# Performance work log

Hardware: AMD Instinct MI355X
Metric: run time of the kernel (lower is better)

The kernel has to match this reference:

```python
import jax, jax.numpy as jnp
import numpy as np

B, C, H, W, N = 32, 256, 56, 56, 1024


def setup_inputs() -> dict:
    key = jax.random.key(0)
    k1, k2, k3, k4 = jax.random.split(key, 4)
    x = jax.random.normal(k1, (B, C, H, W), dtype=jnp.float32)
    W_s = jax.random.normal(k2, (N, H, W), dtype=jnp.float32)
    W_d = jax.random.normal(k3, (N, C, 1, 1), dtype=jnp.float32)
    W_b = jax.random.normal(k4, (1, N), dtype=jnp.float32)
    return {"x": x, "W_s": W_s, "W_d": W_d, "W_b": W_b}


def reference(x, W_s, W_d, W_b):
    # Original: out = einsum('bchw,nhw->bnchw'); per-neuron 1x1 conv with W_d[n]
    # (C -> 1 channel); sum over (c,h,w); add bias. Mathematically:
    #   out[b,n] = sum_{c,h,w} x[b,c,h,w] * W_s[n,h,w] * W_d[n,c] + W_b[0,n]
    # Computed without materializing the (B,N,C,H,W) blow-up:
    y = jnp.einsum('bchw,nhw->bnc', x, W_s)          # spatial contraction
    out = jnp.einsum('bnc,nc->bn', y, W_d[:, :, 0, 0])  # channel contraction
    return out + W_b
```

## Files before the change

kernel.cpp:

```cpp
#include <hip/hip_runtime.h>
#include <stdint.h>


#define K_DIM 3136
#define N_DIM 1024
#define C_DIM 256
#define B_DIM 32
#define M_DIM 8192
#define X_ELEMS (M_DIM * K_DIM)
#define WS_ELEMS (N_DIM * K_DIM)
#define NSTEP 49

typedef __attribute__((ext_vector_type(8))) short short8v;
typedef __attribute__((ext_vector_type(4))) float f32x4;

__device__ __forceinline__ short f2bf(float f) {
  union { float f; unsigned u; } v; v.f = f;
  unsigned r = v.u + 0x7FFFu + ((v.u >> 16) & 1u);
  return (short)(r >> 16);
}

__device__ __forceinline__ void async16(const void* g, void* l) {
  __builtin_amdgcn_global_load_lds(
      (const __attribute__((address_space(1))) unsigned int*)g,
      (__attribute__((address_space(3))) unsigned int*)l, 16, 0, 0);
}

#define XBLK (X_ELEMS / 4096)
#define CVBLK ((X_ELEMS + WS_ELEMS) / 4096)
__global__ __launch_bounds__(256) void convert_bf16_bias(
    const float* __restrict__ x, const float* __restrict__ Ws,
    const float* __restrict__ Wb, short* __restrict__ dst,
    float* __restrict__ out) {
  int bid = blockIdx.x;
  if (bid >= CVBLK) {
    int i = (bid - CVBLK) * 256 + threadIdx.x;
    out[i] = Wb[i & (N_DIM - 1)];
    return;
  }
  const float* src;
  short* d;
  size_t base;
  if (bid < XBLK) {
    src = x; d = dst; base = (size_t)bid * 4096;
  } else {
    src = Ws; d = dst + X_ELEMS; base = (size_t)(bid - XBLK) * 4096;
  }
#pragma unroll
  for (int h = 0; h < 2; ++h) {
    size_t i = base + threadIdx.x * 8 + h * 2048;
    f32x4 v0 = __builtin_nontemporal_load((const f32x4*)(src + i));
    f32x4 v1 = __builtin_nontemporal_load((const f32x4*)(src + i) + 1);
    short8v s;
    s[0] = f2bf(v0.x); s[1] = f2bf(v0.y); s[2] = f2bf(v0.z); s[3] = f2bf(v0.w);
    s[4] = f2bf(v1.x); s[5] = f2bf(v1.y); s[6] = f2bf(v1.z); s[7] = f2bf(v1.w);
    *(short8v*)(d + i) = s;
  }
}


#define VMCNT(N) asm volatile("s_waitcnt vmcnt(" #N ")" ::: "memory")
#define CBAR() asm volatile("" ::: "memory")
#define BARR() { CBAR(); __builtin_amdgcn_s_barrier(); CBAR(); }

#define STAGEA(T) { char* d_ = sm + (((T) & 3) << 15) + (wv << 10);           \
    const short* g_ = Ag + (size_t)(T) * 32;                                  \
    async16(g_, d_);                                                          \
    async16(g_ + (size_t)128 * K_DIM, d_ + 8192); }

#define STAGEB(T) { char* d_ = sm + (((T) & 3) << 15) + 16384 + (wv << 10);   \
    const short* g_ = Bg + (size_t)(T) * 32;                                  \
    async16(g_, d_);                                                          \
    async16(g_ + (size_t)128 * K_DIM, d_ + 8192); }

#define MFQ(F, AV)                                                            \
  acc[F][0] = __builtin_amdgcn_mfma_f32_16x16x32_bf16(AV, b0, acc[F][0], 0, 0, 0); \
  acc[F][1] = __builtin_amdgcn_mfma_f32_16x16x32_bf16(AV, b1, acc[F][1], 0, 0, 0); \
  acc[F][2] = __builtin_amdgcn_mfma_f32_16x16x32_bf16(AV, b2, acc[F][2], 0, 0, 0); \
  acc[F][3] = __builtin_amdgcn_mfma_f32_16x16x32_bf16(AV, b3, acc[F][3], 0, 0, 0);

#define KTILE(T, STG, VMSTMT)                                                 \
  {                                                                           \
    char* sl = sm + (((T) & 3) << 15);                                        \
    if (STG) STAGEA((T) + 3);                                                 \
    short8v b0 = *(const short8v*)(sl + boff);                                \
    short8v b1 = *(const short8v*)(sl + boff + 1024);                         \
    short8v b2 = *(const short8v*)(sl + boff + 2048);                         \
    short8v b3 = *(const short8v*)(sl + boff + 3072);                         \
    short8v a0 = *(const short8v*)(sl + aoff);                                \
    short8v a1 = *(const short8v*)(sl + aoff + 1024);                         \
    short8v a2 = *(const short8v*)(sl + aoff + 2048);                         \
    short8v a3 = *(const short8v*)(sl + aoff + 3072);                         \
    BARR();                                                                   \
    __builtin_amdgcn_s_setprio(1);                                            \
    MFQ(0, a0) MFQ(1, a1) MFQ(2, a2) MFQ(3, a3)                               \
    __builtin_amdgcn_s_setprio(0);                                            \
    BARR();                                                                   \
    if (STG) STAGEB((T) + 3);                                                 \
    a0 = *(const short8v*)(sl + aoff + 4096);                                 \
    a1 = *(const short8v*)(sl + aoff + 5120);                                 \
    a2 = *(const short8v*)(sl + aoff + 6144);                                 \
    a3 = *(const short8v*)(sl + aoff + 7168);                                 \
    VMSTMT;                                                                   \
    __builtin_amdgcn_sched_barrier(0);                                        \
    BARR();                                                                   \
    __builtin_amdgcn_s_setprio(1);                                            \
    MFQ(4, a0) MFQ(5, a1) MFQ(6, a2) MFQ(7, a3)                               \
    __builtin_amdgcn_s_setprio(0);                                            \
    BARR();                                                                   \
  }

__global__ __launch_bounds__(512, 2) void gemm_fused(
    const short* __restrict__ Abf, const short* __restrict__ Bbf,
    const float* __restrict__ Wd, float* __restrict__ out) {
  __shared__ __align__(16) char sm[131072];

  const int bid = blockIdx.x;
  const int xcd = bid & 7;
  const int nt = xcd >> 1;
  const int z = xcd & 1;
  const int mt = bid >> 3;
  const int kt0 = z * NSTEP;

  const int tid = threadIdx.x;
  const int lane = tid & 63;
  const int wv = tid >> 6;
  const int r = lane & 15;
  const int q = lane >> 4;
  const int wm = wv >> 2, wn = wv & 3;

  const int srow = wv * 16 + (lane >> 2);
  const int sk8 = (lane & 3) ^ ((lane >> 3) & 3);
  const short* Ag = Abf + (size_t)(mt * 256 + srow) * K_DIM + kt0 * 32 + sk8 * 8;
  const short* Bg = Bbf + (size_t)(nt * 256 + srow) * K_DIM + kt0 * 32 + sk8 * 8;

  const int swz = (q ^ ((r >> 1) & 3)) << 4;
  const int aoff = (wm * 128 + r) * 64 + swz;
  const int boff = 16384 + (wn * 64 + r) * 64 + swz;

  f32x4 acc[8][4];
#pragma unroll
  for (int i = 0; i < 8; ++i)
#pragma unroll
    for (int j = 0; j < 4; ++j) acc[i][j] = (f32x4)0.0f;

  STAGEA(0) STAGEB(0) STAGEA(1) STAGEB(1) STAGEA(2) STAGEB(2)
  VMCNT(8);
  BARR();

#pragma unroll 1
  for (int t = 0; t < NSTEP - 3; ++t) KTILE(t, 1, VMCNT(8));
  KTILE(NSTEP - 3, 0, VMCNT(4));
  KTILE(NSTEP - 2, 0, VMCNT(0));
  KTILE(NSTEP - 1, 0, (void)0);

#pragma unroll
  for (int j = 0; j < 4; ++j) {
    const int n_g = nt * 256 + wn * 64 + 16 * j + r;
    float p = 0.0f;
#pragma unroll
    for (int i = 0; i < 8; ++i) {
      const int c_l = wm * 128 + 16 * i + 4 * q;
      const float4 wd = *(const float4*)(Wd + (size_t)n_g * C_DIM + c_l);
      p += acc[i][j].x * wd.x + acc[i][j].y * wd.y + acc[i][j].z * wd.z +
           acc[i][j].w * wd.w;
    }
    p += __shfl_xor(p, 16, 64);
    p += __shfl_xor(p, 32, 64);
    if (q == 0) atomicAdd(&out[(size_t)mt * N_DIM + n_g], p);
  }
}

extern "C" void kernel_launch(void* const* d_in, const int* in_sizes, int n_in,
                              void* d_out, int out_size, void* d_ws, size_t ws_size,
                              hipStream_t stream) {
  const float* x = (const float*)d_in[0];
  const float* Ws = (const float*)d_in[1];
  const float* Wd = (const float*)d_in[2];
  const float* Wb = (const float*)d_in[3];
  float* out = (float*)d_out;
  short* xbf = (short*)d_ws;

  convert_bf16_bias<<<dim3(CVBLK + 128), dim3(256), 0, stream>>>(x, Ws, Wb, xbf, out);
  gemm_fused<<<dim3(32 * 4 * 2), dim3(512), 0, stream>>>(xbf, xbf + X_ELEMS, Wd, out);
}
```

Baseline: 212.9 us.

## Fuse x fp32-to-bf16 conversion into GEMM A-tile loading via registers

The separate pre-pass that turned all of x into bf16 in workspace is removed. The GEMM now loads fp32 x rows directly into registers, converts them to bf16 and writes them into swizzled LDS, while B still arrives by async global-to-LDS loads. This drops a full write and re-read of the bf16 copy of x (about 51 MB). In exchange the A tile is loaded at twice the bytes per tile, the software pipeline uses register double-buffering, and the main loop carries more VALU work.

Result: slower. 235.5 us (+10.6%).

```diff
diff --git a/kernel.cpp b/kernel.cpp
--- a/kernel.cpp
+++ b/kernel.cpp
@@ -7,7 +7,6 @@
 #define C_DIM 256
 #define B_DIM 32
 #define M_DIM 8192
-#define X_ELEMS (M_DIM * K_DIM)
 #define WS_ELEMS (N_DIM * K_DIM)
 #define NSTEP 49
 
@@ -26,47 +25,54 @@
       (__attribute__((address_space(3))) unsigned int*)l, 16, 0, 0);
 }
 
-#define XBLK (X_ELEMS / 4096)
-#define CVBLK ((X_ELEMS + WS_ELEMS) / 4096)
-__global__ __launch_bounds__(256) void convert_bf16_bias(
-    const float* __restrict__ x, const float* __restrict__ Ws,
-    const float* __restrict__ Wb, short* __restrict__ dst,
-    float* __restrict__ out) {
+#define WSBLK (WS_ELEMS / 4096)
+__global__ __launch_bounds__(256) void convert_ws_bias(
+    const float* __restrict__ Ws, const float* __restrict__ Wb,
+    short* __restrict__ dst, float* __restrict__ out) {
   int bid = blockIdx.x;
-  if (bid >= CVBLK) {
-    int i = (bid - CVBLK) * 256 + threadIdx.x;
+  if (bid >= WSBLK) {
+    int i = (bid - WSBLK) * 256 + threadIdx.x;
     out[i] = Wb[i & (N_DIM - 1)];
     return;
   }
-  const float* src;
-  short* d;
-  size_t base;
-  if (bid < XBLK) {
-    src = x; d = dst; base = (size_t)bid * 4096;
-  } else {
-    src = Ws; d = dst + X_ELEMS; base = (size_t)(bid - XBLK) * 4096;
-  }
+  size_t base = (size_t)bid * 4096;
 #pragma unroll
   for (int h = 0; h < 2; ++h) {
     size_t i = base + threadIdx.x * 8 + h * 2048;
-    f32x4 v0 = __builtin_nontemporal_load((const f32x4*)(src + i));
-    f32x4 v1 = __builtin_nontemporal_load((const f32x4*)(src + i) + 1);
+    f32x4 v0 = __builtin_nontemporal_load((const f32x4*)(Ws + i));
+    f32x4 v1 = __builtin_nontemporal_load((const f32x4*)(Ws + i) + 1);
     short8v s;
     s[0] = f2bf(v0.x); s[1] = f2bf(v0.y); s[2] = f2bf(v0.z); s[3] = f2bf(v0.w);
     s[4] = f2bf(v1.x); s[5] = f2bf(v1.y); s[6] = f2bf(v1.z); s[7] = f2bf(v1.w);
-    *(short8v*)(d + i) = s;
+    *(short8v*)(dst + i) = s;
   }
 }
 
 
 #define VMCNT(N) asm volatile("s_waitcnt vmcnt(" #N ")" ::: "memory")
+#define LGKM0() asm volatile("s_waitcnt lgkmcnt(0)" ::: "memory")
 #define CBAR() asm volatile("" ::: "memory")
 #define BARR() { CBAR(); __builtin_amdgcn_s_barrier(); CBAR(); }
 
-#define STAGEA(T) { char* d_ = sm + (((T) & 3) << 15) + (wv << 10);           \
-    const short* g_ = Ag + (size_t)(T) * 32;                                  \
-    async16(g_, d_);                                                          \
-    async16(g_ + (size_t)128 * K_DIM, d_ + 8192); }
+#define AISSUE(T, R0, R1, R2, R3) {                                           \
+    const f32x4* p_ = (const f32x4*)(Axp + (size_t)(T) * 32);                 \
+    R0 = p_[0]; R1 = p_[1]; R2 = p_[2]; R3 = p_[3];                           \
+    __builtin_amdgcn_sched_barrier(0); }
+
+#define ACVT(T, R0, R1, R2, R3) {                                             \
+    short8v lo_, hi_;                                                         \
+    lo_[0] = f2bf(R0[0]); lo_[1] = f2bf(R0[1]);                               \
+    lo_[2] = f2bf(R0[2]); lo_[3] = f2bf(R0[3]);                               \
+    lo_[4] = f2bf(R1[0]); lo_[5] = f2bf(R1[1]);                               \
+    lo_[6] = f2bf(R1[2]); lo_[7] = f2bf(R1[3]);                               \
+    hi_[0] = f2bf(R2[0]); hi_[1] = f2bf(R2[1]);                               \
+    hi_[2] = f2bf(R2[2]); hi_[3] = f2bf(R2[3]);                               \
+    hi_[4] = f2bf(R3[0]); hi_[5] = f2bf(R3[1]);                               \
+    hi_[6] = f2bf(R3[2]); hi_[7] = f2bf(R3[3]);                               \
+    char* sb_ = sm + (((T) & 3) << 15);                                       \
+    *(short8v*)(sb_ + aw0) = lo_;                                             \
+    *(short8v*)(sb_ + aw1) = hi_;                                             \
+    CBAR(); }
 
 #define STAGEB(T) { char* d_ = sm + (((T) & 3) << 15) + 16384 + (wv << 10);   \
     const short* g_ = Bg + (size_t)(T) * 32;                                  \
@@ -79,10 +85,10 @@
   acc[F][2] = __builtin_amdgcn_mfma_f32_16x16x32_bf16(AV, b2, acc[F][2], 0, 0, 0); \
   acc[F][3] = __builtin_amdgcn_mfma_f32_16x16x32_bf16(AV, b3, acc[F][3], 0, 0, 0);
 
-#define KTILE(T, STG, VMSTMT)                                                 \
+#define KTILE(T, ISS, CVT, BDM)                                               \
   {                                                                           \
     char* sl = sm + (((T) & 3) << 15);                                        \
-    if (STG) STAGEA((T) + 3);                                                 \
+    ISS                                                                       \
     short8v b0 = *(const short8v*)(sl + boff);                                \
     short8v b1 = *(const short8v*)(sl + boff + 1024);                         \
     short8v b2 = *(const short8v*)(sl + boff + 2048);                         \
@@ -96,13 +102,12 @@
     MFQ(0, a0) MFQ(1, a1) MFQ(2, a2) MFQ(3, a3)                               \
     __builtin_amdgcn_s_setprio(0);                                            \
     BARR();                                                                   \
-    if (STG) STAGEB((T) + 3);                                                 \
+    CVT                                                                       \
+    BDM                                                                       \
     a0 = *(const short8v*)(sl + aoff + 4096);                                 \
     a1 = *(const short8v*)(sl + aoff + 5120);                                 \
     a2 = *(const short8v*)(sl + aoff + 6144);                                 \
     a3 = *(const short8v*)(sl + aoff + 7168);                                 \
-    VMSTMT;                                                                   \
-    __builtin_amdgcn_sched_barrier(0);                                        \
     BARR();                                                                   \
     __builtin_amdgcn_s_setprio(1);                                            \
     MFQ(4, a0) MFQ(5, a1) MFQ(6, a2) MFQ(7, a3)                               \
@@ -111,7 +116,7 @@
   }
 
 __global__ __launch_bounds__(512, 2) void gemm_fused(
-    const short* __restrict__ Abf, const short* __restrict__ Bbf,
+    const float* __restrict__ Ax, const short* __restrict__ Bbf,
     const float* __restrict__ Wd, float* __restrict__ out) {
   __shared__ __align__(16) char sm[131072];
 
@@ -129,9 +134,15 @@
   const int q = lane >> 4;
   const int wm = wv >> 2, wn = wv & 3;
 
+  const int r_ = tid & 255;
+  const int h_ = tid >> 8;
+  const int s2_ = (r_ >> 1) & 3;
+  const int aw0 = r_ * 64 + ((2 * h_ + 0) ^ s2_) * 16;
+  const int aw1 = r_ * 64 + ((2 * h_ + 1) ^ s2_) * 16;
+  const float* Axp = Ax + (size_t)(mt * 256 + r_) * K_DIM + kt0 * 32 + h_ * 16;
+
   const int srow = wv * 16 + (lane >> 2);
   const int sk8 = (lane & 3) ^ ((lane >> 3) & 3);
-  const short* Ag = Abf + (size_t)(mt * 256 + srow) * K_DIM + kt0 * 32 + sk8 * 8;
   const short* Bg = Bbf + (size_t)(nt * 256 + srow) * K_DIM + kt0 * 32 + sk8 * 8;
 
   const int swz = (q ^ ((r >> 1) & 3)) << 4;
@@ -144,15 +155,31 @@
 #pragma unroll
     for (int j = 0; j < 4; ++j) acc[i][j] = (f32x4)0.0f;
 
-  STAGEA(0) STAGEB(0) STAGEA(1) STAGEB(1) STAGEA(2) STAGEB(2)
-  VMCNT(8);
+  f32x4 ra0, ra1, ra2, ra3;
+  f32x4 rb0, rb1, rb2, rb3;
+
+  AISSUE(0, ra0, ra1, ra2, ra3)
+  AISSUE(1, rb0, rb1, rb2, rb3)
+  STAGEB(0) STAGEB(1)
+  ACVT(0, ra0, ra1, ra2, ra3)
+  ACVT(1, rb0, rb1, rb2, rb3)
+  AISSUE(2, ra0, ra1, ra2, ra3)
+  STAGEB(2)
+  VMCNT(6);
+  LGKM0();
   BARR();
 
 #pragma unroll 1
-  for (int t = 0; t < NSTEP - 3; ++t) KTILE(t, 1, VMCNT(8));
-  KTILE(NSTEP - 3, 0, VMCNT(4));
-  KTILE(NSTEP - 2, 0, VMCNT(0));
-  KTILE(NSTEP - 1, 0, (void)0);
+  for (int u = 0; u < 23; ++u) {
+    const int te = 2 * u;
+    KTILE(te, AISSUE(te + 3, rb0, rb1, rb2, rb3),
+          ACVT(te + 2, ra0, ra1, ra2, ra3), STAGEB(te + 3))
+    KTILE(te + 1, AISSUE(te + 4, ra0, ra1, ra2, ra3),
+          ACVT(te + 3, rb0, rb1, rb2, rb3), STAGEB(te + 4))
+  }
+  KTILE(46, , ACVT(48, ra0, ra1, ra2, ra3) VMCNT(0);, )
+  KTILE(47, , , )
+  KTILE(48, , , )
 
 #pragma unroll
   for (int j = 0; j < 4; ++j) {
@@ -179,8 +206,8 @@
   const float* Wd = (const float*)d_in[2];
   const float* Wb = (const float*)d_in[3];
   float* out = (float*)d_out;
-  short* xbf = (short*)d_ws;
-
-  convert_bf16_bias<<<dim3(CVBLK + 128), dim3(256), 0, stream>>>(x, Ws, Wb, xbf, out);
-  gemm_fused<<<dim3(32 * 4 * 2), dim3(512), 0, stream>>>(xbf, xbf + X_ELEMS, Wd, out);
-}
+  short* wsbf = (short*)d_ws;
+
+  convert_ws_bias<<<dim3(WSBLK + 128), dim3(256), 0, stream>>>(Ws, Wb, wsbf, out);
+  gemm_fused<<<dim3(32 * 4 * 2), dim3(512), 0, stream>>>(x, wsbf, Wd, out);
+}
```

## Switch GEMM to 32x32x16 MFMA with register double-buffered LDS reads

Applied to the files above, without the earlier changes.

Replaces the 16x16x32 bf16 MFMA tiling with 32x32x16 MFMAs, giving each wave a 4x2 grid of 32x32 accumulators. The main loop is restructured to prefetch the next half-tile's LDS fragments into a second register set while the current cluster runs, and uses a single barrier per k-tile instead of four. The A and B async stages are merged into one STAGE macro. The aim is fewer LDS reads per flop and less barrier stall, at the cost of a different swizzle and register pressure under the 2-blocks-per-CU launch bound.

Result: slower. 217.3 us (+2.1%).

```diff
diff --git a/kernel.cpp b/kernel.cpp
--- a/kernel.cpp
+++ b/kernel.cpp
@@ -13,6 +13,7 @@
 
 typedef __attribute__((ext_vector_type(8))) short short8v;
 typedef __attribute__((ext_vector_type(4))) float f32x4;
+typedef __attribute__((ext_vector_type(16))) float f32x16;
 
 __device__ __forceinline__ short f2bf(float f) {
   union { float f; unsigned u; } v; v.f = f;
@@ -60,54 +61,69 @@
 
 
 #define VMCNT(N) asm volatile("s_waitcnt vmcnt(" #N ")" ::: "memory")
+#define LGKM0() asm volatile("s_waitcnt lgkmcnt(0)" ::: "memory")
+#define SB0() __builtin_amdgcn_sched_barrier(0)
 #define CBAR() asm volatile("" ::: "memory")
 #define BARR() { CBAR(); __builtin_amdgcn_s_barrier(); CBAR(); }
 
-#define STAGEA(T) { char* d_ = sm + (((T) & 3) << 15) + (wv << 10);           \
-    const short* g_ = Ag + (size_t)(T) * 32;                                  \
-    async16(g_, d_);                                                          \
-    async16(g_ + (size_t)128 * K_DIM, d_ + 8192); }
-
-#define STAGEB(T) { char* d_ = sm + (((T) & 3) << 15) + 16384 + (wv << 10);   \
-    const short* g_ = Bg + (size_t)(T) * 32;                                  \
-    async16(g_, d_);                                                          \
-    async16(g_ + (size_t)128 * K_DIM, d_ + 8192); }
-
-#define MFQ(F, AV)                                                            \
-  acc[F][0] = __builtin_amdgcn_mfma_f32_16x16x32_bf16(AV, b0, acc[F][0], 0, 0, 0); \
-  acc[F][1] = __builtin_amdgcn_mfma_f32_16x16x32_bf16(AV, b1, acc[F][1], 0, 0, 0); \
-  acc[F][2] = __builtin_amdgcn_mfma_f32_16x16x32_bf16(AV, b2, acc[F][2], 0, 0, 0); \
-  acc[F][3] = __builtin_amdgcn_mfma_f32_16x16x32_bf16(AV, b3, acc[F][3], 0, 0, 0);
-
-#define KTILE(T, STG, VMSTMT)                                                 \
+#define STAGE(T) {                                                            \
+    char* da_ = sm + (((T) & 3) << 15) + (wv << 10);                          \
+    const short* ga_ = Ag + (size_t)(T) * 32;                                 \
+    async16(ga_, da_);                                                        \
+    async16(ga_ + (size_t)128 * K_DIM, da_ + 8192);                           \
+    const short* gb_ = Bg + (size_t)(T) * 32;                                 \
+    async16(gb_, da_ + 16384);                                                \
+    async16(gb_ + (size_t)128 * K_DIM, da_ + 24576); }
+
+#define M32(A, B, C) __builtin_amdgcn_mfma_f32_32x32x16_bf16(A, B, C, 0, 0, 0)
+
+#define CLUSTF                                                                \
+  acc[0][0]=M32(fa0,fb0,acc[0][0]); acc[1][0]=M32(fa1,fb0,acc[1][0]);         \
+  acc[2][0]=M32(fa2,fb0,acc[2][0]); acc[3][0]=M32(fa3,fb0,acc[3][0]);         \
+  acc[0][1]=M32(fa0,fb1,acc[0][1]); acc[1][1]=M32(fa1,fb1,acc[1][1]);         \
+  acc[2][1]=M32(fa2,fb1,acc[2][1]); acc[3][1]=M32(fa3,fb1,acc[3][1]);
+
+#define CLUSTG                                                                \
+  acc[0][0]=M32(ga0,gb0,acc[0][0]); acc[1][0]=M32(ga1,gb0,acc[1][0]);         \
+  acc[2][0]=M32(ga2,gb0,acc[2][0]); acc[3][0]=M32(ga3,gb0,acc[3][0]);         \
+  acc[0][1]=M32(ga0,gb1,acc[0][1]); acc[1][1]=M32(ga1,gb1,acc[1][1]);         \
+  acc[2][1]=M32(ga2,gb1,acc[2][1]); acc[3][1]=M32(ga3,gb1,acc[3][1]);
+
+#define RDF(SL) {                                                             \
+    fa0 = *(const short8v*)((SL) + aoff);                                     \
+    fa1 = *(const short8v*)((SL) + aoff + 2048);                              \
+    fa2 = *(const short8v*)((SL) + aoff + 4096);                              \
+    fa3 = *(const short8v*)((SL) + aoff + 6144);                              \
+    fb0 = *(const short8v*)((SL) + boff);                                     \
+    fb1 = *(const short8v*)((SL) + boff + 2048); }
+
+#define RDG(SL) {                                                             \
+    ga0 = *(const short8v*)((SL) + aoffx);                                    \
+    ga1 = *(const short8v*)((SL) + aoffx + 2048);                             \
+    ga2 = *(const short8v*)((SL) + aoffx + 4096);                             \
+    ga3 = *(const short8v*)((SL) + aoffx + 6144);                             \
+    gb0 = *(const short8v*)((SL) + boffx);                                    \
+    gb1 = *(const short8v*)((SL) + boffx + 2048); }
+
+#define KT(T, DOSTG, VMS)                                                     \
   {                                                                           \
     char* sl = sm + (((T) & 3) << 15);                                        \
-    if (STG) STAGEA((T) + 3);                                                 \
-    short8v b0 = *(const short8v*)(sl + boff);                                \
-    short8v b1 = *(const short8v*)(sl + boff + 1024);                         \
-    short8v b2 = *(const short8v*)(sl + boff + 2048);                         \
-    short8v b3 = *(const short8v*)(sl + boff + 3072);                         \
-    short8v a0 = *(const short8v*)(sl + aoff);                                \
-    short8v a1 = *(const short8v*)(sl + aoff + 1024);                         \
-    short8v a2 = *(const short8v*)(sl + aoff + 2048);                         \
-    short8v a3 = *(const short8v*)(sl + aoff + 3072);                         \
+    char* sn = sm + ((((T) + 1) & 3) << 15);                                  \
+    if (DOSTG) STAGE((T) + 3);                                                \
+    RDG(sl);                                                                  \
+    SB0();                                                                    \
+    __builtin_amdgcn_s_setprio(1);                                            \
+    CLUSTF;                                                                   \
+    __builtin_amdgcn_s_setprio(0);                                            \
+    LGKM0();                                                                  \
+    SB0();                                                                    \
+    VMS;                                                                      \
     BARR();                                                                   \
+    RDF(sn);                                                                  \
+    SB0();                                                                    \
     __builtin_amdgcn_s_setprio(1);                                            \
-    MFQ(0, a0) MFQ(1, a1) MFQ(2, a2) MFQ(3, a3)                               \
+    CLUSTG;                                                                   \
     __builtin_amdgcn_s_setprio(0);                                            \
-    BARR();                                                                   \
-    if (STG) STAGEB((T) + 3);                                                 \
-    a0 = *(const short8v*)(sl + aoff + 4096);                                 \
-    a1 = *(const short8v*)(sl + aoff + 5120);                                 \
-    a2 = *(const short8v*)(sl + aoff + 6144);                                 \
-    a3 = *(const short8v*)(sl + aoff + 7168);                                 \
-    VMSTMT;                                                                   \
-    __builtin_amdgcn_sched_barrier(0);                                        \
-    BARR();                                                                   \
-    __builtin_amdgcn_s_setprio(1);                                            \
-    MFQ(4, a0) MFQ(5, a1) MFQ(6, a2) MFQ(7, a3)                               \
-    __builtin_amdgcn_s_setprio(0);                                            \
-    BARR();                                                                   \
   }
 
 __global__ __launch_bounds__(512, 2) void gemm_fused(
@@ -125,8 +141,8 @@
   const int tid = threadIdx.x;
   const int lane = tid & 63;
   const int wv = tid >> 6;
-  const int r = lane & 15;
-  const int q = lane >> 4;
+  const int l31 = lane & 31;
+  const int q2 = lane >> 5;
   const int wm = wv >> 2, wn = wv & 3;
 
   const int srow = wv * 16 + (lane >> 2);
@@ -134,40 +150,49 @@
   const short* Ag = Abf + (size_t)(mt * 256 + srow) * K_DIM + kt0 * 32 + sk8 * 8;
   const short* Bg = Bbf + (size_t)(nt * 256 + srow) * K_DIM + kt0 * 32 + sk8 * 8;
 
-  const int swz = (q ^ ((r >> 1) & 3)) << 4;
-  const int aoff = (wm * 128 + r) * 64 + swz;
-  const int boff = 16384 + (wn * 64 + r) * 64 + swz;
-
-  f32x4 acc[8][4];
-#pragma unroll
-  for (int i = 0; i < 8; ++i)
-#pragma unroll
-    for (int j = 0; j < 4; ++j) acc[i][j] = (f32x4)0.0f;
-
-  STAGEA(0) STAGEB(0) STAGEA(1) STAGEB(1) STAGEA(2) STAGEB(2)
+  const int sA = (l31 >> 1) & 3;
+  const int aoff = (wm * 128 + l31) * 64 + ((q2 ^ sA) << 4);
+  const int boff = 16384 + (wn * 64 + l31) * 64 + ((q2 ^ sA) << 4);
+  const int aoffx = aoff ^ 32;
+  const int boffx = boff ^ 32;
+
+  f32x16 acc[4][2];
+#pragma unroll
+  for (int i = 0; i < 4; ++i)
+#pragma unroll
+    for (int j = 0; j < 2; ++j) acc[i][j] = (f32x16)0.0f;
+
+  short8v fa0, fa1, fa2, fa3, fb0, fb1;
+  short8v ga0, ga1, ga2, ga3, gb0, gb1;
+
+  STAGE(0) STAGE(1) STAGE(2)
   VMCNT(8);
   BARR();
+  RDF(sm);
+  SB0();
 
 #pragma unroll 1
-  for (int t = 0; t < NSTEP - 3; ++t) KTILE(t, 1, VMCNT(8));
-  KTILE(NSTEP - 3, 0, VMCNT(4));
-  KTILE(NSTEP - 2, 0, VMCNT(0));
-  KTILE(NSTEP - 1, 0, (void)0);
-
-#pragma unroll
-  for (int j = 0; j < 4; ++j) {
-    const int n_g = nt * 256 + wn * 64 + 16 * j + r;
+  for (int t = 0; t < NSTEP - 3; ++t) KT(t, 1, VMCNT(8));
+  KT(NSTEP - 3, 0, VMCNT(4));
+  KT(NSTEP - 2, 0, VMCNT(0));
+  KT(NSTEP - 1, 0, (void)0);
+
+#pragma unroll
+  for (int j = 0; j < 2; ++j) {
+    const int n_g = nt * 256 + wn * 64 + j * 32 + l31;
     float p = 0.0f;
 #pragma unroll
-    for (int i = 0; i < 8; ++i) {
-      const int c_l = wm * 128 + 16 * i + 4 * q;
-      const float4 wd = *(const float4*)(Wd + (size_t)n_g * C_DIM + c_l);
-      p += acc[i][j].x * wd.x + acc[i][j].y * wd.y + acc[i][j].z * wd.z +
-           acc[i][j].w * wd.w;
+    for (int i = 0; i < 4; ++i) {
+      const int cb = wm * 128 + i * 32 + 4 * q2;
+#pragma unroll
+      for (int g = 0; g < 4; ++g) {
+        const float4 wd = *(const float4*)(Wd + (size_t)n_g * C_DIM + cb + 8 * g);
+        p += acc[i][j][4 * g + 0] * wd.x + acc[i][j][4 * g + 1] * wd.y +
+             acc[i][j][4 * g + 2] * wd.z + acc[i][j][4 * g + 3] * wd.w;
+      }
     }
-    p += __shfl_xor(p, 16, 64);
     p += __shfl_xor(p, 32, 64);
-    if (q == 0) atomicAdd(&out[(size_t)mt * N_DIM + n_g], p);
+    if (q2 == 0) atomicAdd(&out[(size_t)mt * N_DIM + n_g], p);
   }
 }
 
```
